# Performance work log

Measured on AMD Instinct MI355X. Metric: run time of the kernel, lower is better.

## Reference

```python
import jax, jax.numpy as jnp
import numpy as np

D_MODEL = 1024
NUM_HEADS = 16
D_HEAD = D_MODEL // NUM_HEADS
NEG_INF = float(np.finfo(np.float32).min)


def setup_inputs() -> dict:
    key = jax.random.key(0)
    ks = jax.random.split(key, 6)
    B, S = 2, 2048
    q = jax.random.normal(ks[0], (B, S, D_MODEL), dtype=jnp.float32)
    k = jax.random.normal(ks[1], (B, S, D_MODEL), dtype=jnp.float32)
    v = jax.random.normal(ks[2], (B, S, D_MODEL), dtype=jnp.float32)
    # causal boolean mask: True = attend
    attn_mask = jnp.tril(jnp.ones((S, S), dtype=bool))
    # nn.Linear(d_model, d_model, bias=False) weights: [out, in]; y = x @ W.T
    init_scale = 1.0 / np.sqrt(D_MODEL)
    Wq = jax.random.uniform(ks[3], (D_MODEL, D_MODEL), jnp.float32, -init_scale, init_scale)
    Wk = jax.random.uniform(ks[4], (D_MODEL, D_MODEL), jnp.float32, -init_scale, init_scale)
    Wv = jax.random.uniform(ks[5], (D_MODEL, D_MODEL), jnp.float32, -init_scale, init_scale)
    return {"query": q, "key": k, "value": v, "Wq": Wq, "Wk": Wk, "Wv": Wv,
            "attn_mask": attn_mask}


def _split_heads(x):
    # [B, S, D_MODEL] -> [B, H, S, d_head]
    B, S, _ = x.shape
    return x.reshape(B, S, NUM_HEADS, D_HEAD).transpose(0, 2, 1, 3)


def reference(query, key, value, Wq, Wk, Wv, attn_mask):
    B, Sq, _ = query.shape
    Sk = key.shape[1]
    q = _split_heads(query @ Wq.T)   # [B, H, Sq, dh]
    k = _split_heads(key @ Wk.T)     # [B, H, Sk, dh]
    v = _split_heads(value @ Wv.T)   # [B, H, Sk, dh]
    scale = 1.0 / np.sqrt(D_HEAD)
    scores = jnp.einsum('bhqd,bhkd->bhqk', q, k) * scale  # [B, H, Sq, Sk]
    scores = jnp.where(attn_mask[None, None, :, :], scores, NEG_INF)
    attn_weights = jax.nn.softmax(scores, axis=-1)
    ctx = jnp.einsum('bhqk,bhkd->bhqd', attn_weights, v)   # [B, H, Sq, dh]
    context = ctx.transpose(0, 2, 1, 3).reshape(B, Sq, D_MODEL)
    return context, attn_weights
```

## Files before the change

### kernel.cpp

```cpp
#include <hip/hip_runtime.h>
#include <hip/hip_bf16.h>

#define B_ 2
#define H_ 16
#define S_ 2048
#define DH_ 64
#define DM_ 1024
#define BH_ (B_*H_)
#define CTX_ELEMS (B_*S_*DM_)
#define HEAD_ELEMS (S_*DH_)

typedef __attribute__((ext_vector_type(4))) float  f32x4;
typedef __attribute__((ext_vector_type(8))) short  short8;
typedef __attribute__((ext_vector_type(4))) unsigned short ush4;
typedef unsigned short u16;
typedef unsigned int u32;

__device__ __forceinline__ u16 f2bf(float f) {
  union { __hip_bfloat16 h; u16 u; } cv;
  cv.h = __float2bfloat16(f);
  return cv.u;
}
__device__ __forceinline__ float bf2f(u16 u) {
  union { unsigned int i; float f; } cv;
  cv.i = ((unsigned int)u) << 16;
  return cv.f;
}

__device__ __forceinline__ void gload_lds16(const u16* g, u16* l) {
  __builtin_amdgcn_global_load_lds(
      (const __attribute__((address_space(1))) u32*)g,
      (__attribute__((address_space(3))) u32*)l, 16, 0, 0);
}

__global__ __launch_bounds__(256) void convert_all(
    const float* __restrict__ q, const float* __restrict__ k, const float* __restrict__ v,
    const float* __restrict__ wq, const float* __restrict__ wk, const float* __restrict__ wv,
    u16* __restrict__ xb, u16* __restrict__ wb)
{
  const int t = blockIdx.y;
  const float* s; u16* d; int nblk;
  if (t < 3) {
    s = (t == 0) ? wq : (t == 1) ? wk : wv;
    d = wb + (size_t)t * (DM_ * DM_);
    nblk = 512;
  } else {
    s = (t == 3) ? q : (t == 4) ? k : v;
    d = xb + (size_t)(t - 3) * ((size_t)B_ * S_ * DM_);
    nblk = 2048;
  }
  if (blockIdx.x >= nblk) return;
  const int i = (blockIdx.x * 256 + threadIdx.x) * 8;
  f32x4 a = *(const f32x4*)(s + i);
  f32x4 b = *(const f32x4*)(s + i + 4);
  short8 p;
#pragma unroll
  for (int j = 0; j < 4; ++j) { p[j] = (short)f2bf(a[j]); p[4 + j] = (short)f2bf(b[j]); }
  *(short8*)(d + i) = p;
}

__global__ __launch_bounds__(256) void proj_gemm(
    const u16* __restrict__ Xb, const u16* __restrict__ Wb,
    u16* __restrict__ O0, u16* __restrict__ O1, u16* __restrict__ O2)
{
  u16* O = (blockIdx.z == 0) ? O0 : (blockIdx.z == 1) ? O1 : O2;
  const u16* A = Xb + (size_t)blockIdx.z * ((size_t)B_ * S_ * DM_);
  const u16* W = Wb + (size_t)blockIdx.z * (DM_ * DM_);

  const int m0 = blockIdx.x * 128;
  const int n0 = blockIdx.y * 128;

  __shared__ u16 As[128 * 32];
  __shared__ u16 Bs[128 * 32];

  const int tid  = threadIdx.x;
  const int lane = tid & 63;
  const int w    = tid >> 6;
  const int wr   = w >> 1, wc = w & 1;
  const int l15  = lane & 15, l4 = lane >> 4;

  f32x4 acc[4][4];
#pragma unroll
  for (int i = 0; i < 4; ++i)
#pragma unroll
    for (int j = 0; j < 4; ++j) acc[i][j] = (f32x4){0.f, 0.f, 0.f, 0.f};

  const int srow = lane >> 2;
  const int scol = (lane & 3) * 8;
  const int ca = w * 2;
  const u16* ga0 = A + (size_t)(m0 + ca * 16 + srow) * DM_ + scol;
  const u16* ga1 = A + (size_t)(m0 + ca * 16 + 16 + srow) * DM_ + scol;
  const u16* gb0 = W + (size_t)(n0 + ca * 16 + srow) * DM_ + scol;
  const u16* gb1 = W + (size_t)(n0 + ca * 16 + 16 + srow) * DM_ + scol;

  for (int kb = 0; kb < DM_ / 32; ++kb) {
    const int k0 = kb * 32;
    gload_lds16(ga0 + k0, &As[ca * 512]);
    gload_lds16(ga1 + k0, &As[ca * 512 + 512]);
    gload_lds16(gb0 + k0, &Bs[ca * 512]);
    gload_lds16(gb1 + k0, &Bs[ca * 512 + 512]);
    __syncthreads();
    short8 af[4], bfr[4];
#pragma unroll
    for (int i = 0; i < 4; ++i)
      af[i] = *(const short8*)&As[(wr * 64 + i * 16 + l15) * 32 + l4 * 8];
#pragma unroll
    for (int j = 0; j < 4; ++j)
      bfr[j] = *(const short8*)&Bs[(wc * 64 + j * 16 + l15) * 32 + l4 * 8];
#pragma unroll
    for (int i = 0; i < 4; ++i)
#pragma unroll
      for (int j = 0; j < 4; ++j)
        acc[i][j] = __builtin_amdgcn_mfma_f32_16x16x32_bf16(af[i], bfr[j], acc[i][j], 0, 0, 0);
    __syncthreads();
  }

#pragma unroll
  for (int i = 0; i < 4; ++i) {
#pragma unroll
    for (int j = 0; j < 4; ++j) {
#pragma unroll
      for (int r = 0; r < 4; ++r) {
        const int grow = m0 + wr * 64 + i * 16 + l4 * 4 + r;
        const int gcol = n0 + wc * 64 + j * 16 + l15;
        const int b = grow >> 11, s = grow & (S_ - 1);
        const int h = gcol >> 6,  d = gcol & (DH_ - 1);
        O[(size_t)((b << 4) + h) * HEAD_ELEMS + (size_t)s * DH_ + d] = f2bf(acc[i][j][r]);
      }
    }
  }
}

__global__ __launch_bounds__(256) void transpose_v(const u16* __restrict__ vb,
                                                   u16* __restrict__ vt)
{
  __shared__ u16 T[64][72];
  const int bh = blockIdx.y;
  const int s0 = blockIdx.x * 64;
  const int tid = threadIdx.x;
  {
    const int sl = tid >> 2, dof = (tid & 3) * 16;
    const u16* src = vb + (size_t)bh * HEAD_ELEMS + (size_t)(s0 + sl) * DH_ + dof;
    *(short8*)&T[sl][dof]     = *(const short8*)(src);
    *(short8*)&T[sl][dof + 8] = *(const short8*)(src + 8);
  }
  __syncthreads();
  {
    const int dd = tid >> 2, sof = (tid & 3) * 16;
    u16* dst = vt + (size_t)bh * HEAD_ELEMS + (size_t)dd * S_ + s0 + sof;
    short8 t0, t1;
#pragma unroll
    for (int j = 0; j < 8; ++j) t0[j] = (short)T[sof + j][dd];
#pragma unroll
    for (int j = 0; j < 8; ++j) t1[j] = (short)T[sof + 8 + j][dd];
    *(short8*)(dst)     = t0;
    *(short8*)(dst + 8) = t1;
  }
}

#define PROW 2048
#define ATT_SMEM (16 * PROW * 2 + 16 * 4 + 64 * 4)

__global__ __launch_bounds__(256) void attn_kernel(
    const u16* __restrict__ qb, const u16* __restrict__ kb, const u16* __restrict__ vt,
    float* __restrict__ ctx, float* __restrict__ attnw)
{
  extern __shared__ u16 smem[];
  u16* P = smem;
  float* rinv    = (float*)(smem + 16 * PROW);
  float* partial = rinv + 16;

  const int lin = blockIdx.y * 128 + blockIdx.x;
  const int nl  = (lin & 7) * 512 + (lin >> 3);
  const int bh  = nl >> 7;
  const int qtl = nl & 127;
  const int qt  = 127 - qtl;

  const int tid = threadIdx.x;
  const int lane = tid & 63;
  const int w = tid >> 6;
  const int l15 = lane & 15, l4 = lane >> 4;

  const int NCC = ((qt * 16 + 16) + 127) >> 7;
  const int ncols = NCC << 7;

  const u16* Qb = qb + (size_t)bh * HEAD_ELEMS + (size_t)(qt * 16) * DH_;
  const u16* Kb = kb + (size_t)bh * HEAD_ELEMS;
  const u16* Vt = vt + (size_t)bh * HEAD_ELEMS;

  {
    short8 aQ0 = *(const short8*)(Qb + (size_t)l15 * DH_ + l4 * 8);
    short8 aQ1 = *(const short8*)(Qb + (size_t)l15 * DH_ + l4 * 8 + 32);
    const int qrow = l4 * 4;
    const int qabs = qt * 16 + qrow;
    float psum[4] = {0.f, 0.f, 0.f, 0.f};
    for (int ci = 0; ci < NCC; ++ci) {
      const int col0 = (ci << 7) + w * 32;
#pragma unroll
      for (int t = 0; t < 2; ++t) {
        const int ct = col0 + t * 16;
        const u16* kp = Kb + (size_t)(ct + l15) * DH_ + l4 * 8;
        short8 b0 = *(const short8*)(kp);
        short8 b1 = *(const short8*)(kp + 32);
        f32x4 a0 = (f32x4){0.f, 0.f, 0.f, 0.f};
        f32x4 a1 = (f32x4){0.f, 0.f, 0.f, 0.f};
        a0 = __builtin_amdgcn_mfma_f32_16x16x32_bf16(aQ0, b0, a0, 0, 0, 0);
        a1 = __builtin_amdgcn_mfma_f32_16x16x32_bf16(aQ1, b1, a1, 0, 0, 0);
        const f32x4 a = a0 + a1;
        const int cg = ct + l15;
#pragma unroll
        for (int r = 0; r < 4; ++r) {
          const float e = (cg <= qabs + r) ? __expf(a[r] * 0.125f) : 0.f;
          psum[r] += e;
          const int row = qrow + r;
          P[(row << 11) + (cg ^ ((row & 7) << 3))] = f2bf(e);
        }
      }
    }
#pragma unroll
    for (int r = 0; r < 4; ++r) {
      float s = psum[r];
      s += __shfl_xor(s, 1);
      s += __shfl_xor(s, 2);
      s += __shfl_xor(s, 4);
      s += __shfl_xor(s, 8);
      if (l15 == 0) partial[w * 16 + qrow + r] = s;
    }
  }
  __syncthreads();
  if (tid < 16) {
    const float l = partial[tid] + partial[16 + tid] + partial[32 + tid] + partial[48 + tid];
    rinv[tid] = 1.0f / l;
  }
  __syncthreads();

  auto phase2a = [&]() {
    const int row = tid >> 4, sub = tid & 15;
    const float inv = rinv[row];
    const int swz = (row & 7) << 3;
    const u16* prow = P + (row << 11);
    float* orow = attnw + (size_t)bh * ((size_t)S_ * S_) + (size_t)(qt * 16 + row) * S_;
    for (int c4 = sub * 4; c4 < S_; c4 += 64) {
      f32x4 o;
      if (c4 < ncols) {
        ush4 pv = *(const ush4*)(prow + (c4 ^ swz));
        o[0] = bf2f(pv[0]) * inv;
        o[1] = bf2f(pv[1]) * inv;
        o[2] = bf2f(pv[2]) * inv;
        o[3] = bf2f(pv[3]) * inv;
      } else {
        o = (f32x4){0.f, 0.f, 0.f, 0.f};
      }
      __builtin_nontemporal_store(o, (f32x4*)(orow + c4));
    }
  };

  auto phase2b = [&]() {
    const int dq = w;
    f32x4 acc0 = (f32x4){0.f, 0.f, 0.f, 0.f};
    f32x4 acc1 = (f32x4){0.f, 0.f, 0.f, 0.f};
    const u16* vp0 = Vt + (size_t)(dq * 16 + l15) * S_ + l4 * 8;
    const u16* prow = P + (l15 << 11);
    const int swz = (l15 & 7) << 3;
    for (int c = 0; c < ncols; c += 64) {
      short8 ap0 = *(const short8*)(prow + ((c + l4 * 8) ^ swz));
      short8 bv0 = *(const short8*)(vp0 + c);
      acc0 = __builtin_amdgcn_mfma_f32_16x16x32_bf16(ap0, bv0, acc0, 0, 0, 0);
      short8 ap1 = *(const short8*)(prow + ((c + 32 + l4 * 8) ^ swz));
      short8 bv1 = *(const short8*)(vp0 + c + 32);
      acc1 = __builtin_amdgcn_mfma_f32_16x16x32_bf16(ap1, bv1, acc1, 0, 0, 0);
    }
    const f32x4 acc = acc0 + acc1;
    const int b = bh >> 4, h = bh & 15;
#pragma unroll
    for (int r = 0; r < 4; ++r) {
      const int rg = qt * 16 + l4 * 4 + r;
      const float inv = rinv[l4 * 4 + r];
      __builtin_nontemporal_store(acc[r] * inv,
          ctx + (size_t)(b * S_ + rg) * DM_ + h * 64 + dq * 16 + l15);
    }
  };

  if (qtl & 1) { phase2b(); phase2a(); }
  else         { phase2a(); phase2b(); }
}

extern "C" void kernel_launch(void* const* d_in, const int* in_sizes, int n_in,
                              void* d_out, int out_size, void* d_ws, size_t ws_size,
                              hipStream_t stream) {
  const float* q  = (const float*)d_in[0];
  const float* k  = (const float*)d_in[1];
  const float* v  = (const float*)d_in[2];
  const float* Wq = (const float*)d_in[3];
  const float* Wk = (const float*)d_in[4];
  const float* Wv = (const float*)d_in[5];

  float* ctx   = (float*)d_out;
  float* attnw = ctx + CTX_ELEMS;

  u16* wb = (u16*)d_ws;
  u16* qb = wb + (size_t)3 * DM_ * DM_;
  u16* kb = qb + (size_t)BH_ * HEAD_ELEMS;
  u16* vb = kb + (size_t)BH_ * HEAD_ELEMS;
  u16* vt = vb + (size_t)BH_ * HEAD_ELEMS;
  u16* xb = (u16*)attnw;

  hipFuncSetAttribute(reinterpret_cast<const void*>(attn_kernel),
                      hipFuncAttributeMaxDynamicSharedMemorySize, ATT_SMEM);

  convert_all<<<dim3(2048, 6), 256, 0, stream>>>(q, k, v, Wq, Wk, Wv, xb, wb);
  proj_gemm<<<dim3(32, 8, 3), 256, 0, stream>>>(xb, wb, qb, kb, vb);
  transpose_v<<<dim3(32, 32), 256, 0, stream>>>(vb, vt);
  attn_kernel<<<dim3(128, 32), 256, ATT_SMEM, stream>>>(qb, kb, vt, ctx, attnw);
}
```

Measured before the change: 220.2 us.

## Fuse V transpose into projection GEMM and offload causal zero-fill of attention weights

```diff
diff --git a/kernel.cpp b/kernel.cpp
--- a/kernel.cpp
+++ b/kernel.cpp
@@ -8,7 +8,10 @@
 #define DM_ 1024
 #define BH_ (B_*H_)
 #define CTX_ELEMS (B_*S_*DM_)
+#define ATTNW_ELEMS ((size_t)BH_*S_*S_)
+#define OUT_ELEMS ((size_t)CTX_ELEMS + ATTNW_ELEMS)
 #define HEAD_ELEMS (S_*DH_)
+#define XB_ELEMS ((size_t)3*B_*S_*DM_)
 
 typedef __attribute__((ext_vector_type(4))) float  f32x4;
 typedef __attribute__((ext_vector_type(8))) short  short8;
@@ -61,9 +64,9 @@
 
 __global__ __launch_bounds__(256) void proj_gemm(
     const u16* __restrict__ Xb, const u16* __restrict__ Wb,
-    u16* __restrict__ O0, u16* __restrict__ O1, u16* __restrict__ O2)
+    u16* __restrict__ qb, u16* __restrict__ kb, u16* __restrict__ vt,
+    float* __restrict__ attnw)
 {
-  u16* O = (blockIdx.z == 0) ? O0 : (blockIdx.z == 1) ? O1 : O2;
   const u16* A = Xb + (size_t)blockIdx.z * ((size_t)B_ * S_ * DM_);
   const u16* W = Wb + (size_t)blockIdx.z * (DM_ * DM_);
 
@@ -115,46 +118,48 @@
     __syncthreads();
   }
 
-#pragma unroll
-  for (int i = 0; i < 4; ++i) {
-#pragma unroll
-    for (int j = 0; j < 4; ++j) {
-#pragma unroll
-      for (int r = 0; r < 4; ++r) {
-        const int grow = m0 + wr * 64 + i * 16 + l4 * 4 + r;
-        const int gcol = n0 + wc * 64 + j * 16 + l15;
-        const int b = grow >> 11, s = grow & (S_ - 1);
-        const int h = gcol >> 6,  d = gcol & (DH_ - 1);
-        O[(size_t)((b << 4) + h) * HEAD_ELEMS + (size_t)s * DH_ + d] = f2bf(acc[i][j][r]);
-      }
-    }
-  }
-}
-
-__global__ __launch_bounds__(256) void transpose_v(const u16* __restrict__ vb,
-                                                   u16* __restrict__ vt)
-{
-  __shared__ u16 T[64][72];
-  const int bh = blockIdx.y;
-  const int s0 = blockIdx.x * 64;
-  const int tid = threadIdx.x;
+  if (blockIdx.z == 2) {
+#pragma unroll
+    for (int i = 0; i < 4; ++i)
+#pragma unroll
+      for (int j = 0; j < 4; ++j)
+#pragma unroll
+        for (int r = 0; r < 4; ++r) {
+          const int grow = m0 + wr * 64 + i * 16 + l4 * 4 + r;
+          const int gcol = n0 + wc * 64 + j * 16 + l15;
+          const int b = grow >> 11, s = grow & (S_ - 1);
+          const int h = gcol >> 6,  d = gcol & (DH_ - 1);
+          vt[(size_t)((b << 4) + h) * HEAD_ELEMS + (size_t)d * S_ + s] = f2bf(acc[i][j][r]);
+        }
+  } else {
+    u16* O = (blockIdx.z == 0) ? qb : kb;
+#pragma unroll
+    for (int i = 0; i < 4; ++i)
+#pragma unroll
+      for (int j = 0; j < 4; ++j)
+#pragma unroll
+        for (int r = 0; r < 4; ++r) {
+          const int grow = m0 + wr * 64 + i * 16 + l4 * 4 + r;
+          const int gcol = n0 + wc * 64 + j * 16 + l15;
+          const int b = grow >> 11, s = grow & (S_ - 1);
+          const int h = gcol >> 6,  d = gcol & (DH_ - 1);
+          O[(size_t)((b << 4) + h) * HEAD_ELEMS + (size_t)s * DH_ + d] = f2bf(acc[i][j][r]);
+        }
+  }
+
   {
-    const int sl = tid >> 2, dof = (tid & 3) * 16;
-    const u16* src = vb + (size_t)bh * HEAD_ELEMS + (size_t)(s0 + sl) * DH_ + dof;
-    *(short8*)&T[sl][dof]     = *(const short8*)(src);
-    *(short8*)&T[sl][dof + 8] = *(const short8*)(src + 8);
-  }
-  __syncthreads();
-  {
-    const int dd = tid >> 2, sof = (tid & 3) * 16;
-    u16* dst = vt + (size_t)bh * HEAD_ELEMS + (size_t)dd * S_ + s0 + sof;
-    short8 t0, t1;
-#pragma unroll
-    for (int j = 0; j < 8; ++j) t0[j] = (short)T[sof + j][dd];
-#pragma unroll
-    for (int j = 0; j < 8; ++j) t1[j] = (short)T[sof + 8 + j][dd];
-    *(short8*)(dst)     = t0;
-    *(short8*)(dst + 8) = t1;
+    const int p = (blockIdx.z * 8 + blockIdx.y) * 32 + blockIdx.x;
+    const f32x4 z = (f32x4){0.f, 0.f, 0.f, 0.f};
+    const int base = p * 60;
+    for (int rr = 0; rr < 60; ++rr) {
+      const int zrow = base + rr;
+      const int bh = zrow / 1536;
+      const int s  = zrow - bh * 1536;
+      const int nc = ((s >> 7) + 1) << 7;
+      float* orow = attnw + (size_t)bh * ((size_t)S_ * S_) + (size_t)s * S_;
+      for (int c = nc + tid * 4; c < S_; c += 1024)
+        __builtin_nontemporal_store(z, (f32x4*)(orow + c));
+    }
   }
 }
 
@@ -183,6 +188,7 @@
 
   const int NCC = ((qt * 16 + 16) + 127) >> 7;
   const int ncols = NCC << 7;
+  const int qtmax = qt * 16 + 15;
 
   const u16* Qb = qb + (size_t)bh * HEAD_ELEMS + (size_t)(qt * 16) * DH_;
   const u16* Kb = kb + (size_t)bh * HEAD_ELEMS;
@@ -199,21 +205,29 @@
 #pragma unroll
       for (int t = 0; t < 2; ++t) {
         const int ct = col0 + t * 16;
-        const u16* kp = Kb + (size_t)(ct + l15) * DH_ + l4 * 8;
-        short8 b0 = *(const short8*)(kp);
-        short8 b1 = *(const short8*)(kp + 32);
-        f32x4 a0 = (f32x4){0.f, 0.f, 0.f, 0.f};
-        f32x4 a1 = (f32x4){0.f, 0.f, 0.f, 0.f};
-        a0 = __builtin_amdgcn_mfma_f32_16x16x32_bf16(aQ0, b0, a0, 0, 0, 0);
-        a1 = __builtin_amdgcn_mfma_f32_16x16x32_bf16(aQ1, b1, a1, 0, 0, 0);
-        const f32x4 a = a0 + a1;
         const int cg = ct + l15;
-#pragma unroll
-        for (int r = 0; r < 4; ++r) {
-          const float e = (cg <= qabs + r) ? __expf(a[r] * 0.125f) : 0.f;
-          psum[r] += e;
-          const int row = qrow + r;
-          P[(row << 11) + (cg ^ ((row & 7) << 3))] = f2bf(e);
+        if (ct <= qtmax) {
+          const u16* kp = Kb + (size_t)cg * DH_ + l4 * 8;
+          short8 b0 = *(const short8*)(kp);
+          short8 b1 = *(const short8*)(kp + 32);
+          f32x4 a0 = (f32x4){0.f, 0.f, 0.f, 0.f};
+          f32x4 a1 = (f32x4){0.f, 0.f, 0.f, 0.f};
+          a0 = __builtin_amdgcn_mfma_f32_16x16x32_bf16(aQ0, b0, a0, 0, 0, 0);
+          a1 = __builtin_amdgcn_mfma_f32_16x16x32_bf16(aQ1, b1, a1, 0, 0, 0);
+          const f32x4 a = a0 + a1;
+#pragma unroll
+          for (int r = 0; r < 4; ++r) {
+            const float e = (cg <= qabs + r) ? __expf(a[r] * 0.125f) : 0.f;
+            psum[r] += e;
+            const int row = qrow + r;
+            P[(row << 11) + (cg ^ ((row & 7) << 3))] = f2bf(e);
+          }
+        } else {
+#pragma unroll
+          for (int r = 0; r < 4; ++r) {
+            const int row = qrow + r;
+            P[(row << 11) + (cg ^ ((row & 7) << 3))] = 0;
+          }
         }
       }
     }
@@ -235,23 +249,28 @@
   __syncthreads();
 
   auto phase2a = [&]() {
-    const int row = tid >> 4, sub = tid & 15;
-    const float inv = rinv[row];
-    const int swz = (row & 7) << 3;
-    const u16* prow = P + (row << 11);
-    float* orow = attnw + (size_t)bh * ((size_t)S_ * S_) + (size_t)(qt * 16 + row) * S_;
-    for (int c4 = sub * 4; c4 < S_; c4 += 64) {
-      f32x4 o;
-      if (c4 < ncols) {
-        ush4 pv = *(const ush4*)(prow + (c4 ^ swz));
+    const bool do_zeros = (bh >= 30) || (qt >= 96);
+    const f32x4 z = (f32x4){0.f, 0.f, 0.f, 0.f};
+#pragma unroll
+    for (int rr = 0; rr < 4; ++rr) {
+      const int row = rr * 4 + w;
+      const float inv = rinv[row];
+      const int swz = (row & 7) << 3;
+      const u16* prow = P + (row << 11);
+      float* orow = attnw + (size_t)bh * ((size_t)S_ * S_) + (size_t)(qt * 16 + row) * S_;
+      for (int c = lane * 4; c < ncols; c += 256) {
+        ush4 pv = *(const ush4*)(prow + (c ^ swz));
+        f32x4 o;
         o[0] = bf2f(pv[0]) * inv;
         o[1] = bf2f(pv[1]) * inv;
         o[2] = bf2f(pv[2]) * inv;
         o[3] = bf2f(pv[3]) * inv;
-      } else {
-        o = (f32x4){0.f, 0.f, 0.f, 0.f};
+        __builtin_nontemporal_store(o, (f32x4*)(orow + c));
       }
-      __builtin_nontemporal_store(o, (f32x4*)(orow + c4));
+      if (do_zeros) {
+        for (int c = ncols + lane * 4; c < S_; c += 256)
+          __builtin_nontemporal_store(z, (f32x4*)(orow + c));
+      }
     }
   };
 
@@ -301,15 +320,13 @@
   u16* wb = (u16*)d_ws;
   u16* qb = wb + (size_t)3 * DM_ * DM_;
   u16* kb = qb + (size_t)BH_ * HEAD_ELEMS;
-  u16* vb = kb + (size_t)BH_ * HEAD_ELEMS;
-  u16* vt = vb + (size_t)BH_ * HEAD_ELEMS;
-  u16* xb = (u16*)attnw;
+  u16* vt = kb + (size_t)BH_ * HEAD_ELEMS;
+  u16* xb = (u16*)(ctx + (OUT_ELEMS - XB_ELEMS / 2));
 
   hipFuncSetAttribute(reinterpret_cast<const void*>(attn_kernel),
                       hipFuncAttributeMaxDynamicSharedMemorySize, ATT_SMEM);
 
   convert_all<<<dim3(2048, 6), 256, 0, stream>>>(q, k, v, Wq, Wk, Wv, xb, wb);
-  proj_gemm<<<dim3(32, 8, 3), 256, 0, stream>>>(xb, wb, qb, kb, vb);
-  transpose_v<<<dim3(32, 32), 256, 0, stream>>>(vb, vt);
+  proj_gemm<<<dim3(32, 8, 3), 256, 0, stream>>>(xb, wb, qb, kb, vt, attnw);
   attn_kernel<<<dim3(128, 32), 256, ATT_SMEM, stream>>>(qb, kb, vt, ctx, attnw);
 }
```

Result: slower. 247.4 us (+12.3%).
